# Optimization experiments

Hardware: AMD Instinct MI355X
Metric: run time of the kernel (lower is better)

## Reference

```python
import jax, jax.numpy as jnp
import numpy as np


def _conv(x, w, stride, padding):
    # x: [N, Cin, H, W], w: [Cout, Cin, kh, kw]
    return jax.lax.conv_general_dilated(
        x, w, window_strides=(stride, stride), padding=padding,
        dimension_numbers=("NCHW", "OIHW", "NCHW"))


def _reflect_pad1(x):
    return jnp.pad(x, ((0, 0), (0, 0), (1, 1), (1, 1)), mode="reflect")


def setup_inputs() -> dict:
    key = jax.random.key(0)
    k1, k2, k3, k4 = jax.random.split(key, 4)
    B, C, H, W = 16, 3, 512, 512
    NC = 20  # num_channels (intermediate width)
    # xavier-uniform-like scales
    x = jax.random.normal(k1, (B, C, H, W), dtype=jnp.float32)
    w1 = jax.random.normal(k2, (NC, 1, 4, 4), dtype=jnp.float32) * (6.0 / (1 * 16 + NC * 16)) ** 0.5
    w2 = jax.random.normal(k3, (NC, NC, 4, 4), dtype=jnp.float32) * (6.0 / (NC * 16 + NC * 16)) ** 0.5
    w3 = jax.random.normal(k4, (1, NC, 3, 3), dtype=jnp.float32) * (6.0 / (NC * 9 + 1 * 9)) ** 0.5
    return {"x": x, "w1": w1, "w2": w2, "w3": w3}


def reference(x, w1, w2, w3):
    # Original torch code loops over input channels; equivalently fold the
    # channel dim into the batch dim and run the whole pipeline once.
    B, C, H, W = x.shape
    xr = x.reshape(B * C, 1, H, W)
    # stage 1: reflect pad 1 + 4x4 stride-2 conv + relu
    o1 = jax.nn.relu(_conv(_reflect_pad1(xr), w1, 2, "VALID"))  # [B*C, NC, 256, 256]
    # stage 2: reflect pad 1 + 4x4 stride-2 conv + relu
    o2 = jax.nn.relu(_conv(_reflect_pad1(o1), w2, 2, "VALID"))  # [B*C, NC, 128, 128]
    # stage 3: 3x3 conv, zero padding 1, + relu -> 1 channel per input channel
    o3 = jax.nn.relu(_conv(o2, w3, 1, ((1, 1), (1, 1))))        # [B*C, 1, 128, 128]
    Ho, Wo = o3.shape[-2], o3.shape[-1]
    return o3.reshape(B, C, Ho, Wo)
```

## Files before the change

kernel.cpp:

```cpp
#include <hip/hip_runtime.h>


#define NC 20
#define TS 12
#define S1RP 600
#define S1CIN 30
#define SO2 14
#define PS2 196
#define NWG (48 * 121)
#define CPX (NWG / 8)

#define W2F_OFF 256
#define W3_OFF  5376
#define WP_N    5556

typedef _Float16 h2  __attribute__((ext_vector_type(2)));
typedef __fp16   hq2 __attribute__((ext_vector_type(2)));
typedef _Float16 h8  __attribute__((ext_vector_type(8)));
typedef float    f32x16 __attribute__((ext_vector_type(16)));

__device__ __forceinline__ float dot2(unsigned int a, unsigned int b, float c) {
    return __builtin_amdgcn_fdot2(__builtin_bit_cast(h2, a),
                                  __builtin_bit_cast(h2, b), c, false);
}
__device__ __forceinline__ unsigned int packh(float a, float b) {
    _Float16 ha = (_Float16)a, hb = (_Float16)b;
    return (unsigned int)__builtin_bit_cast(unsigned short, ha) |
           ((unsigned int)__builtin_bit_cast(unsigned short, hb) << 16);
}
__device__ __forceinline__ unsigned int pkrtz(float a, float b) {
    hq2 r = __builtin_amdgcn_cvt_pkrtz(a, b);
    return __builtin_bit_cast(unsigned int, r);
}
__device__ __forceinline__ unsigned int pk_relu(unsigned int u) {
    unsigned int r;
    asm("v_pk_max_f16 %0, %1, 0" : "=v"(r) : "v"(u));
    return r;
}
__device__ __forceinline__ int refl256(int q) {
    q = (q < 0) ? -q : q; return (q > 255) ? 510 - q : q;
}
__device__ __forceinline__ int refl512(int q) {
    q = (q < 0) ? -q : q; return (q > 511) ? 1022 - q : q;
}

__global__ __launch_bounds__(256) void pack_weights(
    const float* __restrict__ w1, const float* __restrict__ w2,
    const float* __restrict__ w3, unsigned int* __restrict__ wp)
{
    const int i = blockIdx.x * 256 + threadIdx.x;
    if (i >= WP_N) return;
    if (i < W2F_OFF) {
        const int lane = i >> 2, jp = i & 3;
        const int ch = lane & 31, k0 = (lane >> 5) * 8 + 2 * jp;
        wp[i] = (ch < NC) ? packh(w1[ch * 16 + k0], w1[ch * 16 + k0 + 1]) : 0u;
    } else if (i < W3_OFF) {
        const int t = i - W2F_OFF;
        const int cin = t >> 8, r = t & 255;
        const int lane = r >> 2, jp = r & 3;
        const int cout = lane & 31;
        const int k0 = (lane >> 5) * 8 + ((jp & 1) << 2) + ((jp >> 1) << 1);
        wp[i] = (cout < NC) ? packh(w2[(cout * NC + cin) * 16 + k0],
                                    w2[(cout * NC + cin) * 16 + k0 + 1]) : 0u;
    } else {
        const int t = i - W3_OFF;
        const int c = t / 9;
        const int r = t - c * 9;
        const int di = r / 3, wh = r - di * 3;
        const float* row = w3 + c * 9 + di * 3;
        float a, b;
        if (wh == 0)      { a = row[0]; b = row[1]; }
        else if (wh == 1) { a = row[2]; b = 0.f;    }
        else              { a = 0.f;    b = row[2]; }
        wp[i] = packh(a, b);
    }
}

__device__ __forceinline__ void load_taps(
    const float* __restrict__ xi, int t0, int h, int wv, int kh,
    bool rowEdge, bool colEdge, int vb, int v0, int v1, int v2, int v3,
    unsigned int xw[4][4])
{
    #pragma unroll
    for (int i = 0; i < 4; ++i) {
        const int c = wv + 4 * i;
        const int t = t0 + 14 * h + c;
        int rlo, rhi;
        if (!rowEdge) {
            rlo = 2 * t - 3 + 2 * kh;
            rhi = rlo + 1;
        } else {
            const int mr = refl256(t - 1);
            const int rb = 2 * mr - 1 + 2 * kh;
            rlo = refl512(rb);
            rhi = refl512(rb + 1);
        }
        const float* __restrict__ plo = xi + rlo * 512;
        const float* __restrict__ phi = xi + rhi * 512;
        float f0, f1, f2, f3, f4, f5, f6, f7;
        if (!colEdge) {
            f0 = plo[vb]; f1 = plo[vb + 1]; f2 = plo[vb + 2]; f3 = plo[vb + 3];
            f4 = phi[vb]; f5 = phi[vb + 1]; f6 = phi[vb + 2]; f7 = phi[vb + 3];
        } else {
            f0 = plo[v0]; f1 = plo[v1]; f2 = plo[v2]; f3 = plo[v3];
            f4 = phi[v0]; f5 = phi[v1]; f6 = phi[v2]; f7 = phi[v3];
        }
        xw[i][0] = pkrtz(f0, f1); xw[i][1] = pkrtz(f2, f3);
        xw[i][2] = pkrtz(f4, f5); xw[i][3] = pkrtz(f6, f7);
    }
}

__global__ __launch_bounds__(256, 6) void ds_fused(
    const float* __restrict__ x,
    const unsigned int* __restrict__ wp,
    float* __restrict__ out)
{
    __shared__ __attribute__((aligned(16))) unsigned short s_o1[8 * S1RP * 2];
    __shared__ __attribute__((aligned(16))) unsigned short s_o2[NC * PS2];

    const int rawb = blockIdx.x;
    const int bid  = (rawb & 7) * CPX + (rawb >> 3);

    const int img  = bid / 121;
    const int t121 = bid - img * 121;
    const int ty   = t121 / 11;
    const int tx   = t121 - ty * 11;
    const int y0   = ty * TS;
    const int x0   = tx * TS;
    const int tid  = threadIdx.x;
    const int lane = tid & 63;
    const int wv   = tid >> 6;
    const int l31  = lane & 31;
    const int kh   = lane >> 5;

    const float* __restrict__ xi = x + (size_t)img * (512 * 512);
    const uint4* __restrict__ w1f = (const uint4*)wp;
    const uint4* __restrict__ w2f = (const uint4*)(wp + W2F_OFF);
    const unsigned int* __restrict__ w3p = wp + W3_OFF;

    const int t0 = 2 * y0 - 2;
    const int s0 = 2 * x0 - 2;

    const int sA = s0 + l31;
    const bool rowEdge = (ty == 0) || (ty == 10);
    const bool colEdge = (tx == 0) || (tx == 10);
    const bool interior = !rowEdge && !colEdge;
    const int vb = 2 * sA - 3;
    int v0 = 0, v1 = 0, v2 = 0, v3 = 0;
    if (colEdge) {
        const int n2 = refl256(sA - 1);
        const int vbb = 2 * n2 - 1;
        v0 = refl512(vbb);     v1 = refl512(vbb + 1);
        v2 = refl512(vbb + 2); v3 = refl512(vbb + 3);
    }
    const h8 w1frag = __builtin_bit_cast(h8, w1f[lane]);

    const int q  = 32 * wv + l31;
    const int qc = (q < 98) ? q : 0;
    const int li = (qc * 2341) >> 15;
    const int jl = qc - li * 14;
    const int offR = (li + kh) * (S1RP / 2) + jl;

    unsigned int* const s1d = (unsigned int*)s_o1;
    const uint2* const so1v = (const uint2*)s_o1;

    unsigned int xw0[4][4];
    load_taps(xi, t0, 0, wv, kh, rowEdge, colEdge, vb, v0, v1, v2, v3, xw0);

    #pragma unroll
    for (int i = 0; i < 4; ++i) {
        const int c = wv + 4 * i;
        uint4 aw; aw.x = xw0[i][0]; aw.y = xw0[i][1];
                  aw.z = xw0[i][2]; aw.w = xw0[i][3];
        f32x16 o = {};
        o = __builtin_amdgcn_mfma_f32_32x32x16_f16(
                __builtin_bit_cast(h8, aw), w1frag, o, 0, 0, 0);
        if (l31 < NC) {
            unsigned int* wr = s1d + (c >> 1) * S1RP + l31 * S1CIN + (c & 1);
            const int kb = 4 * kh;
            wr[kb + 0]  = pk_relu(pkrtz(o[0],  o[1]));
            wr[kb + 2]  = pk_relu(pkrtz(o[2],  o[3]));
            wr[kb + 8]  = pk_relu(pkrtz(o[4],  o[5]));
            wr[kb + 10] = pk_relu(pkrtz(o[6],  o[7]));
            wr[kb + 16] = pk_relu(pkrtz(o[8],  o[9]));
            wr[kb + 18] = pk_relu(pkrtz(o[10], o[11]));
            wr[kb + 24] = pk_relu(pkrtz(o[12], o[13]));
            if (kh == 0)
                wr[kb + 26] = pk_relu(pkrtz(o[14], o[15]));
        }
    }

    unsigned int xw1[4][4];
    load_taps(xi, t0, 1, wv, kh, rowEdge, colEdge, vb, v0, v1, v2, v3, xw1);

    #pragma unroll
    for (int h = 0; h < 2; ++h) {
        if (h == 1) {
            __syncthreads();
            #pragma unroll
            for (int i = 0; i < 4; ++i) {
                const int c = wv + 4 * i;
                uint4 aw; aw.x = xw1[i][0]; aw.y = xw1[i][1];
                          aw.z = xw1[i][2]; aw.w = xw1[i][3];
                f32x16 o = {};
                o = __builtin_amdgcn_mfma_f32_32x32x16_f16(
                        __builtin_bit_cast(h8, aw), w1frag, o, 0, 0, 0);
                if (l31 < NC) {
                    unsigned int* wr =
                        s1d + (c >> 1) * S1RP + l31 * S1CIN + (c & 1);
                    const int kb = 4 * kh;
                    wr[kb + 0]  = pk_relu(pkrtz(o[0],  o[1]));
                    wr[kb + 2]  = pk_relu(pkrtz(o[2],  o[3]));
                    wr[kb + 8]  = pk_relu(pkrtz(o[4],  o[5]));
                    wr[kb + 10] = pk_relu(pkrtz(o[6],  o[7]));
                    wr[kb + 16] = pk_relu(pkrtz(o[8],  o[9]));
                    wr[kb + 18] = pk_relu(pkrtz(o[10], o[11]));
                    wr[kb + 24] = pk_relu(pkrtz(o[12], o[13]));
                    if (kh == 0)
                        wr[kb + 26] = pk_relu(pkrtz(o[14], o[15]));
                }
            }
        }
        __syncthreads();

        f32x16 acc = {};
        #pragma unroll 4
        for (int cin = 0; cin < NC; ++cin) {
            const uint4 bw = w2f[cin * 64 + lane];
            const uint2* pA = so1v + cin * (S1CIN / 2) + offR;
            const uint2 lo = pA[0];
            const uint2 hi = pA[1];
            uint4 aw; aw.x = lo.x; aw.y = lo.y; aw.z = hi.x; aw.w = hi.y;
            acc = __builtin_amdgcn_mfma_f32_32x32x16_f16(
                      __builtin_bit_cast(h8, aw),
                      __builtin_bit_cast(h8, bw), acc, 0, 0, 0);
        }

        if (l31 < NC) {
            unsigned short* bp = &s_o2[l31 * PS2 + 98 * h + 32 * wv + 4 * kh];
            if (interior) {
                #pragma unroll
                for (int j = 0; j < 4; ++j) {
                    const int Q = 32 * wv + 4 * kh + 8 * j;
                    if (Q < 98)
                        *(unsigned int*)(bp + 8 * j) =
                            pk_relu(pkrtz(acc[4 * j], acc[4 * j + 1]));
                    if (Q + 2 < 98)
                        *(unsigned int*)(bp + 8 * j + 2) =
                            pk_relu(pkrtz(acc[4 * j + 2], acc[4 * j + 3]));
                }
            } else {
                #pragma unroll
                for (int d = 0; d < 8; ++d) {
                    const int jj = d >> 1, ss = d & 1;
                    const int Qd = 32 * wv + 4 * kh + 8 * jj + 2 * ss;
                    if (Qd < 98) {
                        const int li2 = (Qd * 2341) >> 15;
                        const int jl2 = Qd - li2 * 14;
                        const int oi  = y0 - 1 + 7 * h + li2;
                        const int oj  = x0 - 1 + jl2;
                        const bool rok = (oi >= 0) && (oi < 128);
                        const unsigned int m =
                            (rok && oj >= 0 && oj < 128 ? 0x0000FFFFu : 0u) |
                            (rok && oj + 1 < 128        ? 0xFFFF0000u : 0u);
                        *(unsigned int*)(bp + 8 * jj + 2 * ss) =
                            pk_relu(pkrtz(acc[4 * jj + 2 * ss],
                                          acc[4 * jj + 2 * ss + 1])) & m;
                    }
                }
            }
        }
    }
    __syncthreads();

    if (tid < TS * TS) {
        const int oy = tid / TS;
        const int ox = tid - oy * TS;
        const int e  = ox & ~1;
        const int par = ox & 1;
        const unsigned int shp = (unsigned int)(par << 4);
        const unsigned int* wsel = w3p + 1 + par;
        float a0 = 0.f, a1 = 0.f, a2 = 0.f;
        #pragma unroll
        for (int c = 0; c < NC; ++c) {
            const unsigned short* pl = &s_o2[c * PS2 + oy * SO2 + e];
            #pragma unroll
            for (int di = 0; di < 3; ++di) {
                const unsigned int* row = (const unsigned int*)(pl + di * SO2);
                const unsigned int d0 = row[0];
                const unsigned int d1 = row[1];
                const unsigned int u0 = __builtin_amdgcn_alignbit(d1, d0, shp);
                const unsigned int wa = w3p[c * 9 + di * 3 + 0];
                const unsigned int wz = wsel[c * 9 + di * 3];
                float& aR = (di == 0) ? a0 : ((di == 1) ? a1 : a2);
                aR = dot2(u0, wa, aR);
                aR = dot2(d1, wz, aR);
            }
        }
        const float accc = a0 + a1 + a2;
        const int gy = y0 + oy, gx = x0 + ox;
        if (gy < 128 && gx < 128)
            out[(size_t)img * (128 * 128) + gy * 128 + gx] = fmaxf(accc, 0.f);
    }
}

extern "C" void kernel_launch(void* const* d_in, const int* in_sizes, int n_in,
                              void* d_out, int out_size, void* d_ws, size_t ws_size,
                              hipStream_t stream) {
    const float* x  = (const float*)d_in[0];
    const float* w1 = (const float*)d_in[1];
    const float* w2 = (const float*)d_in[2];
    const float* w3 = (const float*)d_in[3];
    unsigned int* wp = (unsigned int*)d_ws;
    float* out = (float*)d_out;
    pack_weights<<<dim3((WP_N + 255) / 256), dim3(256), 0, stream>>>(w1, w2, w3, wp);
    ds_fused<<<dim3(NWG), dim3(256), 0, stream>>>(x, wp, out);
}
```

Baseline: 165.1 us.

## Keep both stage-1 halves in LDS and run stage 2 in one pass

Stage-1 output for both halves of the tile now stays in a larger LDS buffer, with overlapping rows shared between them, so the second half no longer waits on a separate barrier-and-recompute phase. Both x tap loads are issued up front and the stage-2 weights are preloaded into registers. Stage 2 then accumulates two independent MFMA chains in a single fully unrolled loop. In exchange, LDS use per block and register pressure rise, and the launch bound drops occupancy from 6 to 3 blocks per CU.

```diff
diff --git a/kernel.cpp b/kernel.cpp
--- a/kernel.cpp
+++ b/kernel.cpp
@@ -110,12 +110,12 @@
     }
 }
 
-__global__ __launch_bounds__(256, 6) void ds_fused(
+__global__ __launch_bounds__(256, 3) void ds_fused(
     const float* __restrict__ x,
     const unsigned int* __restrict__ wp,
     float* __restrict__ out)
 {
-    __shared__ __attribute__((aligned(16))) unsigned short s_o1[8 * S1RP * 2];
+    __shared__ __attribute__((aligned(16))) unsigned short s_o1[15 * S1RP * 2];
     __shared__ __attribute__((aligned(16))) unsigned short s_o2[NC * PS2];
 
     const int rawb = blockIdx.x;
@@ -159,13 +159,19 @@
     const int qc = (q < 98) ? q : 0;
     const int li = (qc * 2341) >> 15;
     const int jl = qc - li * 14;
-    const int offR = (li + kh) * (S1RP / 2) + jl;
+    const int offR0 = (li + kh) * (S1RP / 2) + jl;
+    const int offR1 = offR0 + 7 * (S1RP / 2);
 
     unsigned int* const s1d = (unsigned int*)s_o1;
     const uint2* const so1v = (const uint2*)s_o1;
 
-    unsigned int xw0[4][4];
+    unsigned int xw0[4][4], xw1[4][4];
     load_taps(xi, t0, 0, wv, kh, rowEdge, colEdge, vb, v0, v1, v2, v3, xw0);
+    load_taps(xi, t0, 1, wv, kh, rowEdge, colEdge, vb, v0, v1, v2, v3, xw1);
+
+    uint4 bwr[NC];
+    #pragma unroll
+    for (int cin = 0; cin < NC; ++cin) bwr[cin] = w2f[cin * 64 + lane];
 
     #pragma unroll
     for (int i = 0; i < 4; ++i) {
@@ -189,54 +195,52 @@
                 wr[kb + 26] = pk_relu(pkrtz(o[14], o[15]));
         }
     }
-
-    unsigned int xw1[4][4];
-    load_taps(xi, t0, 1, wv, kh, rowEdge, colEdge, vb, v0, v1, v2, v3, xw1);
-
-    #pragma unroll
-    for (int h = 0; h < 2; ++h) {
-        if (h == 1) {
-            __syncthreads();
-            #pragma unroll
-            for (int i = 0; i < 4; ++i) {
-                const int c = wv + 4 * i;
-                uint4 aw; aw.x = xw1[i][0]; aw.y = xw1[i][1];
-                          aw.z = xw1[i][2]; aw.w = xw1[i][3];
-                f32x16 o = {};
-                o = __builtin_amdgcn_mfma_f32_32x32x16_f16(
-                        __builtin_bit_cast(h8, aw), w1frag, o, 0, 0, 0);
-                if (l31 < NC) {
-                    unsigned int* wr =
-                        s1d + (c >> 1) * S1RP + l31 * S1CIN + (c & 1);
-                    const int kb = 4 * kh;
-                    wr[kb + 0]  = pk_relu(pkrtz(o[0],  o[1]));
-                    wr[kb + 2]  = pk_relu(pkrtz(o[2],  o[3]));
-                    wr[kb + 8]  = pk_relu(pkrtz(o[4],  o[5]));
-                    wr[kb + 10] = pk_relu(pkrtz(o[6],  o[7]));
-                    wr[kb + 16] = pk_relu(pkrtz(o[8],  o[9]));
-                    wr[kb + 18] = pk_relu(pkrtz(o[10], o[11]));
-                    wr[kb + 24] = pk_relu(pkrtz(o[12], o[13]));
-                    if (kh == 0)
-                        wr[kb + 26] = pk_relu(pkrtz(o[14], o[15]));
-                }
-            }
-        }
-        __syncthreads();
-
-        f32x16 acc = {};
-        #pragma unroll 4
-        for (int cin = 0; cin < NC; ++cin) {
-            const uint4 bw = w2f[cin * 64 + lane];
-            const uint2* pA = so1v + cin * (S1CIN / 2) + offR;
-            const uint2 lo = pA[0];
-            const uint2 hi = pA[1];
-            uint4 aw; aw.x = lo.x; aw.y = lo.y; aw.z = hi.x; aw.w = hi.y;
-            acc = __builtin_amdgcn_mfma_f32_32x32x16_f16(
-                      __builtin_bit_cast(h8, aw),
-                      __builtin_bit_cast(h8, bw), acc, 0, 0, 0);
-        }
-
-        if (l31 < NC) {
+    #pragma unroll
+    for (int i = 0; i < 4; ++i) {
+        const int c = wv + 4 * i;
+        uint4 aw; aw.x = xw1[i][0]; aw.y = xw1[i][1];
+                  aw.z = xw1[i][2]; aw.w = xw1[i][3];
+        f32x16 o = {};
+        o = __builtin_amdgcn_mfma_f32_32x32x16_f16(
+                __builtin_bit_cast(h8, aw), w1frag, o, 0, 0, 0);
+        if (l31 < NC && c >= 2) {
+            unsigned int* wr =
+                s1d + (7 + (c >> 1)) * S1RP + l31 * S1CIN + (c & 1);
+            const int kb = 4 * kh;
+            wr[kb + 0]  = pk_relu(pkrtz(o[0],  o[1]));
+            wr[kb + 2]  = pk_relu(pkrtz(o[2],  o[3]));
+            wr[kb + 8]  = pk_relu(pkrtz(o[4],  o[5]));
+            wr[kb + 10] = pk_relu(pkrtz(o[6],  o[7]));
+            wr[kb + 16] = pk_relu(pkrtz(o[8],  o[9]));
+            wr[kb + 18] = pk_relu(pkrtz(o[10], o[11]));
+            wr[kb + 24] = pk_relu(pkrtz(o[12], o[13]));
+            if (kh == 0)
+                wr[kb + 26] = pk_relu(pkrtz(o[14], o[15]));
+        }
+    }
+    __syncthreads();
+
+    f32x16 acc0 = {}, acc1 = {};
+    #pragma unroll
+    for (int cin = 0; cin < NC; ++cin) {
+        const uint2* pA0 = so1v + cin * (S1CIN / 2) + offR0;
+        const uint2* pA1 = so1v + cin * (S1CIN / 2) + offR1;
+        const uint2 lo0 = pA0[0], hi0 = pA0[1];
+        const uint2 lo1 = pA1[0], hi1 = pA1[1];
+        uint4 aw0; aw0.x = lo0.x; aw0.y = lo0.y; aw0.z = hi0.x; aw0.w = hi0.y;
+        uint4 aw1; aw1.x = lo1.x; aw1.y = lo1.y; aw1.z = hi1.x; aw1.w = hi1.y;
+        acc0 = __builtin_amdgcn_mfma_f32_32x32x16_f16(
+                   __builtin_bit_cast(h8, aw0),
+                   __builtin_bit_cast(h8, bwr[cin]), acc0, 0, 0, 0);
+        acc1 = __builtin_amdgcn_mfma_f32_32x32x16_f16(
+                   __builtin_bit_cast(h8, aw1),
+                   __builtin_bit_cast(h8, bwr[cin]), acc1, 0, 0, 0);
+    }
+
+    if (l31 < NC) {
+        #pragma unroll
+        for (int h = 0; h < 2; ++h) {
+            const f32x16& acc = h ? acc1 : acc0;
             unsigned short* bp = &s_o2[l31 * PS2 + 98 * h + 32 * wv + 4 * kh];
             if (interior) {
                 #pragma unroll
```

New measurement: 155.4 us, median of 2. -5.9%, faster.
